# Kernel tuning notes

Hardware: AMD Instinct MI355X
Metric: run time of the kernel (lower is better)

The kernel has to match this reference:

```python
import jax, jax.numpy as jnp
import numpy as np

B, S, NI = 8, 1024, 1024      # batch, seq_len, n_inputs
L, H, P = 128, 128, 64        # n_latents, hidden=n_inputs//8, prototype_dim
EPS_PROTO = 1e-4              # self.epsilon
BN_EPS = 1e-5                 # torch BatchNorm1d default eps


def setup_inputs() -> dict:
    key = jax.random.key(0)
    ks = jax.random.split(key, 4)
    return {
        "x": jax.random.normal(ks[0], (B, S, NI), jnp.float32),
        "W1": jax.random.normal(ks[1], (L, H, NI), jnp.float32) * 0.02,
        "b1": jnp.zeros((L, H), jnp.float32),
        "gamma": jnp.ones((L, H), jnp.float32),
        "beta": jnp.zeros((L, H), jnp.float32),
        "run_mean": jnp.zeros((L, H), jnp.float32),
        "run_var": jnp.ones((L, H), jnp.float32),
        "W2": jax.random.normal(ks[2], (L, P, H), jnp.float32) * 0.02,
        "b2": jnp.zeros((L, P), jnp.float32),
        "prototypes": jax.random.normal(ks[3], (L, P), jnp.float32) * 0.02,
    }


def reference(x, W1, b1, gamma, beta, run_mean, run_var, W2, b2, prototypes):
    Bb, Ss, _ = x.shape
    xf = x.reshape(Bb * Ss, NI)                       # [T, NI]
    # grouped first Linear over all latents at once: [T, L, H]
    h = jnp.einsum('ti,lhi->tlh', xf, W1) + b1
    # Dropout is identity in eval; BatchNorm1d in eval mode (running stats)
    h = (h - run_mean) * jax.lax.rsqrt(run_var + BN_EPS) * gamma + beta
    h = jax.nn.relu(h)
    # grouped second Linear: [T, L, P]
    enc = jnp.einsum('tlh,lph->tlp', h, W2) + b2
    # prototype L2-distance activation
    l2s = jnp.sum((enc - prototypes) ** 2, axis=-1)   # [T, L]
    raw = jnp.log((l2s + 1.0) / (l2s + EPS_PROTO))
    act = raw / jnp.log(1.0 / EPS_PROTO) * 300.0 - 100.0
    return act.reshape(Bb, Ss, L)
```

## Files before the change

kernel.cpp:

```cpp
#include <hip/hip_runtime.h>


#define NTOK 8192
#define NI   1024
#define NL   128
#define NH   128
#define NP   64

typedef __bf16 bf16x8 __attribute__((ext_vector_type(8)));
typedef float f32x4 __attribute__((ext_vector_type(4)));
typedef int   i32x4 __attribute__((ext_vector_type(4)));

static __device__ __forceinline__ unsigned short f2bf(float f) {
  union { float f; unsigned int u; } v; v.f = f;
  const unsigned int u = v.u;
  return (unsigned short)((u + 0x7fffu + ((u >> 16) & 1u)) >> 16);
}

__global__ void cvt_f32_bf16(const float* __restrict__ in,
                             unsigned short* __restrict__ out, int n8) {
  const int i = blockIdx.x * blockDim.x + threadIdx.x;
  if (i >= n8) return;
  const float4* p = (const float4*)in;
  const float4 a = p[2 * i], b = p[2 * i + 1];
  unsigned short v[8] __attribute__((aligned(16))) = {
      f2bf(a.x), f2bf(a.y), f2bf(a.z), f2bf(a.w),
      f2bf(b.x), f2bf(b.y), f2bf(b.z), f2bf(b.w)};
  ((uint4*)out)[i] = *(const uint4*)v;
}

__global__ void quant_rows_i8_dual(const float* __restrict__ x,
                                   const float* __restrict__ w1,
                                   signed char* __restrict__ xq,
                                   signed char* __restrict__ w1q,
                                   float* __restrict__ sx,
                                   float* __restrict__ sw) {
  const int row = blockIdx.x * 4 + (threadIdx.x >> 6);
  const int lane = threadIdx.x & 63;
  const float* src;
  unsigned int* dst;
  float* sp;
  if (row < NTOK) {
    src = x + (size_t)row * 1024;
    dst = (unsigned int*)(xq + (size_t)row * 1024);
    sp  = sx + row;
  } else {
    const int r = row - NTOK;
    src = w1 + (size_t)r * 1024;
    dst = (unsigned int*)(w1q + (size_t)r * 1024);
    sp  = sw + r;
  }
  const float4* s4 = (const float4*)src;
  float4 v[4];
  float m = 0.f;
#pragma unroll
  for (int j = 0; j < 4; ++j) {
    v[j] = s4[lane + 64 * j];
    m = fmaxf(m, fmaxf(fmaxf(fabsf(v[j].x), fabsf(v[j].y)),
                       fmaxf(fabsf(v[j].z), fabsf(v[j].w))));
  }
#pragma unroll
  for (int s = 1; s < 64; s <<= 1) m = fmaxf(m, __shfl_xor(m, s));
  m = fmaxf(m, 1e-20f);
  const float inv = 127.0f / m;
  if (lane == 0) *sp = m * (1.0f / 127.0f);
#pragma unroll
  for (int j = 0; j < 4; ++j) {
    const int a = (int)rintf(fminf(127.f, fmaxf(-127.f, v[j].x * inv)));
    const int b = (int)rintf(fminf(127.f, fmaxf(-127.f, v[j].y * inv)));
    const int c = (int)rintf(fminf(127.f, fmaxf(-127.f, v[j].z * inv)));
    const int d = (int)rintf(fminf(127.f, fmaxf(-127.f, v[j].w * inv)));
    dst[lane + 64 * j] = (unsigned)(a & 255) | ((unsigned)(b & 255) << 8) |
                         ((unsigned)(c & 255) << 16) | ((unsigned)(d & 255) << 24);
  }
}

static __device__ __forceinline__ void async16(const void* g, void* l) {
  __builtin_amdgcn_global_load_lds(
      (const __attribute__((address_space(1))) unsigned int*)g,
      (__attribute__((address_space(3))) unsigned int*)l, 16, 0, 0);
}

__global__ __launch_bounds__(256, 2) void proto_fused(
    const signed char* __restrict__ xq,
    const signed char* __restrict__ w1q,
    const unsigned short* __restrict__ w2b,
    const float* __restrict__ sx,
    const float* __restrict__ sw,
    const float* __restrict__ b1,
    const float* __restrict__ gamma, const float* __restrict__ beta,
    const float* __restrict__ rmean, const float* __restrict__ rvar,
    const float* __restrict__ b2,
    const float* __restrict__ protos,
    float* __restrict__ out)
{
  __shared__ __attribute__((aligned(128))) char smem[65536];
  const int tid  = threadIdx.x;
  const int wave = tid >> 6;
  const int lane = tid & 63;
  const int l15  = lane & 15;
  const int l4   = lane >> 4;
  const int wr   = wave >> 1;
  const int wc   = wave & 1;

  const int id    = blockIdx.x;
  const int xcd   = id & 7;
  const int local = id >> 3;
  const int chunk = local >> 7;
  const int wi    = local & 127;
  const int tt    = chunk * 8 + (wi & 7);
  const int lat   = xcd * 16 + (wi >> 3);
  const int t0    = tt * 128;

  const int srow  = lane >> 3;
  const int scolb = ((lane & 7) ^ srow) * 16;

  const signed char* aB[4];
  const signed char* bB[4];
  int dA[4], dB[4];
#pragma unroll
  for (int j = 0; j < 4; ++j) {
    const int row = wave * 32 + j * 8 + srow;
    aB[j] = xq  + (size_t)(t0 + row) * NI + scolb;
    bB[j] = w1q + (size_t)(lat * NH + row) * NI + scolb;
    dA[j] = (wave * 4 + j) * 1024;
    dB[j] = 16384 + (wave * 4 + j) * 1024;
  }

  i32x4 acc[4][4] = {};

  auto stage = [&](int buf, int ks) {
    const int k0   = ks * 128;
    const int bofs = buf * 32768;
#pragma unroll
    for (int j = 0; j < 4; ++j) {
      async16(aB[j] + k0, smem + bofs + dA[j]);
      async16(bB[j] + k0, smem + bofs + dB[j]);
    }
  };

  stage(0, 0);
  __syncthreads();
  const int rx = l15 & 7;
  int buf = 0;
  for (int ks = 0; ks < 8; ++ks) {
    if (ks + 1 < 8) stage(buf ^ 1, ks + 1);
    const char* Ab = smem + buf * 32768;
    const char* Bb = Ab + 16384;
    i32x4 a[2][4], b[2][4];
#pragma unroll
    for (int kk = 0; kk < 2; ++kk) {
      const int koff = ((kk * 4 + l4) ^ rx) << 4;
#pragma unroll
      for (int m = 0; m < 4; ++m)
        a[kk][m] = *(const i32x4*)(Ab + (wr * 64 + m * 16 + l15) * 128 + koff);
#pragma unroll
      for (int n = 0; n < 4; ++n)
        b[kk][n] = *(const i32x4*)(Bb + (wc * 64 + n * 16 + l15) * 128 + koff);
    }
    __builtin_amdgcn_s_setprio(1);
#pragma unroll
    for (int kk = 0; kk < 2; ++kk)
#pragma unroll
      for (int m = 0; m < 4; ++m)
#pragma unroll
        for (int n = 0; n < 4; ++n)
          acc[m][n] = __builtin_amdgcn_mfma_i32_16x16x64_i8(a[kk][m], b[kk][n], acc[m][n], 0, 0, 0);
    __builtin_amdgcn_s_setprio(0);
    __syncthreads();
    buf ^= 1;
  }

#pragma unroll
  for (int i = 0; i < 4; ++i) {
    const int r = wave * 4 + i * 16 + l4;
    const int c = (lane & 15) ^ (r & 15);
    async16(w2b + (size_t)lat * NP * NH + r * NH + c * 8,
            smem + 32768 + (wave * 64 + i * 256) * 16);
  }

  float sxv[4][4];
#pragma unroll
  for (int m = 0; m < 4; ++m)
#pragma unroll
    for (int r = 0; r < 4; ++r)
      sxv[m][r] = sx[t0 + wr * 64 + m * 16 + l4 * 4 + r];

#pragma unroll
  for (int n = 0; n < 4; ++n) {
    const int hc = wc * 64 + n * 16 + l15;
    const int gi = lat * NH + hc;
    const float sc_ = gamma[gi] * rsqrtf(rvar[gi] + 1e-5f);
    const float Kc  = sw[gi] * sc_;
    const float Cc  = b1[gi] * sc_ + beta[gi] - rmean[gi] * sc_;
    const int cchunk = hc >> 3, cin = (hc & 7) * 2;
#pragma unroll
    for (int m = 0; m < 4; ++m)
#pragma unroll
      for (int r = 0; r < 4; ++r) {
        float v = fmaf((float)acc[m][n][r] * sxv[m][r], Kc, Cc);
        v = v > 0.f ? v : 0.f;
        const int row = wr * 64 + m * 16 + l4 * 4 + r;
        const int pbyte = row * 256 + ((cchunk ^ (l4 * 4 + r)) << 4) + cin;
        *(__bf16*)(smem + pbyte) = (__bf16)v;
      }
  }
  __syncthreads();

  f32x4 acc2[2][4] = {};
#pragma unroll
  for (int kk = 0; kk < 4; ++kk) {
    const int pcsel = kk * 4 + l4;
    bf16x8 a2[2], bw[4];
#pragma unroll
    for (int m = 0; m < 2; ++m) {
      const int row = wave * 32 + m * 16 + l15;
      a2[m] = *(const bf16x8*)(smem + row * 256 + ((pcsel ^ l15) << 4));
    }
#pragma unroll
    for (int n = 0; n < 4; ++n) {
      const int rp = n * 16 + l15;
      bw[n] = *(const bf16x8*)(smem + 32768 + rp * 256 + ((pcsel ^ l15) << 4));
    }
#pragma unroll
    for (int m = 0; m < 2; ++m)
#pragma unroll
      for (int n = 0; n < 4; ++n)
        acc2[m][n] = __builtin_amdgcn_mfma_f32_16x16x32_bf16(a2[m], bw[n], acc2[m][n], 0, 0, 0);
  }

  float pb[4], pp[4];
#pragma unroll
  for (int n = 0; n < 4; ++n) {
    const int p = n * 16 + l15;
    pb[n] = b2[lat * NP + p];
    pp[n] = protos[lat * NP + p];
  }
  const float scale2 = 0.69314718056f * 300.0f / logf(10000.0f);
#pragma unroll
  for (int m = 0; m < 2; ++m)
#pragma unroll
    for (int r = 0; r < 4; ++r) {
      float s = 0.f;
#pragma unroll
      for (int n = 0; n < 4; ++n) {
        const float e = acc2[m][n][r] + pb[n] - pp[n];
        s += e * e;
      }
      s += __shfl_xor(s, 1);
      s += __shfl_xor(s, 2);
      s += __shfl_xor(s, 4);
      s += __shfl_xor(s, 8);
      if (l15 == 0) {
        const float a = (__log2f(s + 1.0f) - __log2f(s + 1e-4f)) * scale2 - 100.0f;
        const int trow = wave * 32 + m * 16 + l4 * 4 + r;
        out[(size_t)(t0 + trow) * NL + lat] = a;
      }
    }
}

extern "C" void kernel_launch(void* const* d_in, const int* in_sizes, int n_in,
                              void* d_out, int out_size, void* d_ws, size_t ws_size,
                              hipStream_t stream) {
  const float* x      = (const float*)d_in[0];
  const float* W1     = (const float*)d_in[1];
  const float* b1     = (const float*)d_in[2];
  const float* gamma  = (const float*)d_in[3];
  const float* beta   = (const float*)d_in[4];
  const float* rmean  = (const float*)d_in[5];
  const float* rvar   = (const float*)d_in[6];
  const float* W2     = (const float*)d_in[7];
  const float* b2     = (const float*)d_in[8];
  const float* protos = (const float*)d_in[9];
  float* out = (float*)d_out;

  char* ws = (char*)d_ws;
  signed char*    xq  = (signed char*)ws;
  signed char*    w1q = (signed char*)(ws + (size_t)8 * 1024 * 1024);
  unsigned short* w2b = (unsigned short*)(ws + (size_t)24 * 1024 * 1024);
  float*          sx  = (float*)(ws + (size_t)26 * 1024 * 1024);
  float*          sw  = (float*)(ws + (size_t)26 * 1024 * 1024 + 64 * 1024);

  quant_rows_i8_dual<<<(NTOK + NL * NH) / 4, 256, 0, stream>>>(x, W1, xq, w1q, sx, sw);
  {
    const int n8w2 = NL * NP * NH / 8;
    cvt_f32_bf16<<<(n8w2 + 255) / 256, 256, 0, stream>>>(W2, w2b, n8w2);
  }

  proto_fused<<<dim3(8192), 256, 0, stream>>>(xq, w1q, w2b, sx, sw, b1, gamma, beta,
                                              rmean, rvar, b2, protos, out);
}
```

Baseline: 239.9 us.

## Load X operand directly into registers and shrink LDS for higher occupancy

The int8 X tile for the first GEMM is now loaded straight from global memory into registers in MFMA fragment layout, double-buffered across two register sets. Only the W1 tile is staged through LDS. This halves LDS use to 48KB and raises launch bounds to 3 blocks per CU, aiming for more occupancy and fewer LDS reads. In exchange each wave makes redundant, less coalesced global loads of X, and register pressure rises, which may cause spills at the tighter bound.

```diff
diff --git a/kernel.cpp b/kernel.cpp
--- a/kernel.cpp
+++ b/kernel.cpp
@@ -81,7 +81,7 @@
       (__attribute__((address_space(3))) unsigned int*)l, 16, 0, 0);
 }
 
-__global__ __launch_bounds__(256, 2) void proto_fused(
+__global__ __launch_bounds__(256, 3) void proto_fused(
     const signed char* __restrict__ xq,
     const signed char* __restrict__ w1q,
     const unsigned short* __restrict__ w2b,
@@ -94,7 +94,7 @@
     const float* __restrict__ protos,
     float* __restrict__ out)
 {
-  __shared__ __attribute__((aligned(128))) char smem[65536];
+  __shared__ __attribute__((aligned(128))) char smem[49152];
   const int tid  = threadIdx.x;
   const int wave = tid >> 6;
   const int lane = tid & 63;
@@ -115,61 +115,75 @@
   const int srow  = lane >> 3;
   const int scolb = ((lane & 7) ^ srow) * 16;
 
-  const signed char* aB[4];
   const signed char* bB[4];
-  int dA[4], dB[4];
 #pragma unroll
   for (int j = 0; j < 4; ++j) {
     const int row = wave * 32 + j * 8 + srow;
-    aB[j] = xq  + (size_t)(t0 + row) * NI + scolb;
     bB[j] = w1q + (size_t)(lat * NH + row) * NI + scolb;
-    dA[j] = (wave * 4 + j) * 1024;
-    dB[j] = 16384 + (wave * 4 + j) * 1024;
-  }
+  }
+
+  const signed char* xA[4];
+#pragma unroll
+  for (int m = 0; m < 4; ++m)
+    xA[m] = xq + (size_t)(t0 + wr * 64 + m * 16 + l15) * NI + l4 * 16;
 
   i32x4 acc[4][4] = {};
-
-  auto stage = [&](int buf, int ks) {
-    const int k0   = ks * 128;
-    const int bofs = buf * 32768;
-#pragma unroll
-    for (int j = 0; j < 4; ++j) {
-      async16(aB[j] + k0, smem + bofs + dA[j]);
-      async16(bB[j] + k0, smem + bofs + dB[j]);
+  i32x4 aP[8], aQ[8];
+
+  auto stageB = [&](int ks, int buf) {
+    const int k0 = ks * 128;
+    const int bofs = buf * 16384;
+#pragma unroll
+    for (int j = 0; j < 4; ++j)
+      async16(bB[j] + k0, smem + bofs + (wave * 4 + j) * 1024);
+  };
+
+  const int rx = l15 & 7;
+
+#define LOADA(DST, KS)                                                     \
+  _Pragma("unroll")                                                        \
+  for (int q = 0; q < 8; ++q)                                              \
+    DST[q] = *(const i32x4*)(xA[q & 3] + (KS) * 128 + (q >> 2) * 64);
+
+#define BODY(AF, BUF)                                                      \
+  {                                                                        \
+    _Pragma("unroll")                                                      \
+    for (int kk = 0; kk < 2; ++kk) {                                       \
+      const int koff = ((kk * 4 + l4) ^ rx) << 4;                          \
+      i32x4 b[4];                                                          \
+      _Pragma("unroll")                                                    \
+      for (int n = 0; n < 4; ++n)                                          \
+        b[n] = *(const i32x4*)(smem + (BUF) * 16384 +                      \
+                               (wc * 64 + n * 16 + l15) * 128 + koff);     \
+      __builtin_amdgcn_s_setprio(1);                                       \
+      _Pragma("unroll")                                                    \
+      for (int m = 0; m < 4; ++m)                                          \
+        _Pragma("unroll")                                                  \
+        for (int n = 0; n < 4; ++n)                                        \
+          acc[m][n] = __builtin_amdgcn_mfma_i32_16x16x64_i8(               \
+              AF[kk * 4 + m], b[n], acc[m][n], 0, 0, 0);                   \
+      __builtin_amdgcn_s_setprio(0);                                       \
+    }                                                                      \
+  }
+
+  stageB(0, 0);
+  LOADA(aP, 0);
+  __syncthreads();
+#pragma unroll
+  for (int ks = 0; ks < 8; ks += 2) {
+    if (ks + 1 < 8) stageB(ks + 1, 1);
+    LOADA(aQ, ks + 1);
+    BODY(aP, 0);
+    __syncthreads();
+    if (ks + 2 < 8) {
+      stageB(ks + 2, 0);
+      LOADA(aP, ks + 2);
     }
-  };
-
-  stage(0, 0);
-  __syncthreads();
-  const int rx = l15 & 7;
-  int buf = 0;
-  for (int ks = 0; ks < 8; ++ks) {
-    if (ks + 1 < 8) stage(buf ^ 1, ks + 1);
-    const char* Ab = smem + buf * 32768;
-    const char* Bb = Ab + 16384;
-    i32x4 a[2][4], b[2][4];
-#pragma unroll
-    for (int kk = 0; kk < 2; ++kk) {
-      const int koff = ((kk * 4 + l4) ^ rx) << 4;
-#pragma unroll
-      for (int m = 0; m < 4; ++m)
-        a[kk][m] = *(const i32x4*)(Ab + (wr * 64 + m * 16 + l15) * 128 + koff);
-#pragma unroll
-      for (int n = 0; n < 4; ++n)
-        b[kk][n] = *(const i32x4*)(Bb + (wc * 64 + n * 16 + l15) * 128 + koff);
-    }
-    __builtin_amdgcn_s_setprio(1);
-#pragma unroll
-    for (int kk = 0; kk < 2; ++kk)
-#pragma unroll
-      for (int m = 0; m < 4; ++m)
-#pragma unroll
-        for (int n = 0; n < 4; ++n)
-          acc[m][n] = __builtin_amdgcn_mfma_i32_16x16x64_i8(a[kk][m], b[kk][n], acc[m][n], 0, 0, 0);
-    __builtin_amdgcn_s_setprio(0);
+    BODY(aQ, 1);
     __syncthreads();
-    buf ^= 1;
-  }
+  }
+#undef LOADA
+#undef BODY
 
 #pragma unroll
   for (int i = 0; i < 4; ++i) {
```

Measured after the change: 306.4 us. 1.28x slower.
